# Kernel optimization log

Hardware: AMD Instinct MI355X
Metric: run time of the kernel (lower is better)

Reference implementation:

```python
import jax, jax.numpy as jnp
import numpy as np

WS = 7          # window size
HEADS = 8
SHIFT = WS // 2  # shift=True -> 3
C = 256
KD = C // HEADS  # key_dim = 32
LN_EPS = 1e-3    # keras LayerNormalization default


def setup_inputs() -> dict:
    key = jax.random.key(0)
    ks = jax.random.split(key, 12)
    s = 1.0 / np.sqrt(C)
    x = jax.random.normal(ks[0], (16, 112, 112, C), dtype=jnp.float32)
    wq = jax.random.normal(ks[1], (C, HEADS, KD), dtype=jnp.float32) * s
    bq = jnp.zeros((HEADS, KD), dtype=jnp.float32)
    wk = jax.random.normal(ks[2], (C, HEADS, KD), dtype=jnp.float32) * s
    bk = jnp.zeros((HEADS, KD), dtype=jnp.float32)
    wv = jax.random.normal(ks[3], (C, HEADS, KD), dtype=jnp.float32) * s
    bv = jnp.zeros((HEADS, KD), dtype=jnp.float32)
    wo = jax.random.normal(ks[4], (HEADS, KD, C), dtype=jnp.float32) * s
    bo = jnp.zeros((C,), dtype=jnp.float32)
    gamma = jnp.ones((C,), dtype=jnp.float32)
    beta = jnp.zeros((C,), dtype=jnp.float32)
    return {"x": x, "wq": wq, "bq": bq, "wk": wk, "bk": bk,
            "wv": wv, "bv": bv, "wo": wo, "bo": bo,
            "gamma": gamma, "beta": beta}


def _swin_window_attn(x, wq, bq, wk, bk, wv, bv, wo, bo, gamma, beta):
    b, h, w, c = x.shape
    pad_h = (WS - h % WS) % WS
    pad_w = (WS - w % WS) % WS
    if pad_h or pad_w:
        x = jnp.pad(x, ((0, 0), (0, pad_h), (0, pad_w), (0, 0)))
    hp, wp = h + pad_h, w + pad_w
    if SHIFT > 0:
        x = jnp.roll(x, shift=(-SHIFT, -SHIFT), axis=(1, 2))
    nh, nw = hp // WS, wp // WS
    # window partition: (b, nh, WS, nw, WS, c) -> (b*nh*nw, WS*WS, c)
    win = x.reshape(b, nh, WS, nw, WS, c).transpose(0, 1, 3, 2, 4, 5)
    win = win.reshape(b * nh * nw, WS * WS, c)
    # multi-head attention (keras MHA: query scaled by 1/sqrt(key_dim))
    q = jnp.einsum("nsc,chd->nshd", win, wq) + bq
    k = jnp.einsum("nsc,chd->nshd", win, wk) + bk
    v = jnp.einsum("nsc,chd->nshd", win, wv) + bv
    scores = jnp.einsum("nqhd,nkhd->nhqk", q, k) / jnp.sqrt(jnp.float32(KD)).astype(q.dtype)
    probs = jax.nn.softmax(scores, axis=-1)
    ctx = jnp.einsum("nhqk,nkhd->nqhd", probs, v)
    attn = jnp.einsum("nqhd,hdc->nqc", ctx, wo) + bo
    # residual + LayerNorm
    y = attn + win
    mu = jnp.mean(y, axis=-1, keepdims=True)
    var = jnp.mean(jnp.square(y - mu), axis=-1, keepdims=True)
    y = (y - mu) * jax.lax.rsqrt(var + LN_EPS) * gamma + beta
    # window reverse
    out = y.reshape(b, nh, nw, WS, WS, c).transpose(0, 1, 3, 2, 4, 5)
    out = out.reshape(b, hp, wp, c)
    if SHIFT > 0:
        out = jnp.roll(out, shift=(SHIFT, SHIFT), axis=(1, 2))
    if pad_h or pad_w:
        out = out[:, :h, :w, :]
    return out


def reference(x, wq, bq, wk, bk, wv, bv, wo, bo, gamma, beta):
    return _swin_window_attn(x, wq, bq, wk, bk, wv, bv, wo, bo, gamma, beta)
```

## Files before the change

kernel.cpp:

```cpp
#include <hip/hip_runtime.h>
#include <hip/hip_bf16.h>

typedef __attribute__((ext_vector_type(8))) short short8;
typedef __attribute__((ext_vector_type(4))) short short4v;
typedef __attribute__((ext_vector_type(4))) float float4v;
typedef __attribute__((ext_vector_type(2))) unsigned int uint2v;

#define LDS_BYTES 138272
#define XBF_OFF   0
#define VT_OFF    33792
#define Q_OFF     70656
#define K_OFF     104448
#define CTX_OFF   70656
#define Y_OFF     104448
#define FLAG_OFF  138240

__device__ __forceinline__ unsigned short f2bf_rn(float f) {
    union { __hip_bfloat16 b; unsigned short u; } v;
    v.b = __float2bfloat16(f);
    return v.u;
}
__device__ __forceinline__ unsigned int pk2bf(float a, float b) {
    union { __hip_bfloat162 h; unsigned int u; } v;
    v.h = __float22bfloat162_rn(make_float2(a, b));
    return v.u;
}
__device__ __forceinline__ float bf2f(unsigned short h) {
    union { unsigned int u; float f; } v; v.u = ((unsigned int)h) << 16;
    return v.f;
}
union U8 { unsigned int u[4]; short8 s; };

__global__ void prep_weights(const float* __restrict__ wq, const float* __restrict__ wk,
                             const float* __restrict__ wv, const float* __restrict__ wo,
                             unsigned short* __restrict__ wfrag) {
    int tid = blockIdx.x * 256 + threadIdx.x;
    if (tid >= 4 * 65536) return;
    int m = tid >> 16;
    int e = tid & 65535;
    int j = e & 7;
    int lane = (e >> 3) & 63;
    int nt2 = (e >> 9) & 15;
    int ks = e >> 13;
    int c = ks * 32 + (lane >> 4) * 8 + j;
    int o = nt2 * 16 + (lane & 15);
    const float* W = (m == 0) ? wq : (m == 1) ? wk : (m == 2) ? wv : wo;
    wfrag[tid] = f2bf_rn(W[c * 256 + o]);
}

__global__ __launch_bounds__(1024, 4) void swin_fused(
    const float* __restrict__ x,
    const unsigned short* __restrict__ wfrag,
    const float* __restrict__ bq, const float* __restrict__ bk,
    const float* __restrict__ bv, const float* __restrict__ bo,
    const float* __restrict__ gamma, const float* __restrict__ beta,
    float* __restrict__ out)
{
    extern __shared__ char smem[];
    const int tid = threadIdx.x;
    const int w    = tid >> 6;
    const int h    = w & 7;
    const int half = w >> 3;
    const int l   = tid & 63;
    const int l15 = l & 15;
    const int l4  = l >> 4;
    const int nt2 = 2 * h + half;

    const int blk = blockIdx.x;
    const int bb  = blk >> 8;
    const int wh  = (blk >> 4) & 15;
    const int ww  = blk & 15;

    const unsigned short* wqf = wfrag;
    const unsigned short* wkf = wfrag + 65536;
    const unsigned short* wvf = wfrag + 2 * 65536;
    const int woff0 = (nt2 * 64 + l) * 8;
    short8 bq0 = *(const short8*)(wqf + woff0);
    short8 bk0 = *(const short8*)(wkf + woff0);
    short8 bv0 = *(const short8*)(wvf + woff0);

    unsigned short* Xbf = (unsigned short*)(smem + XBF_OFF);

    if (tid < 8) ((int*)(smem + FLAG_OFF))[tid] = 0;
    for (int idx = tid; idx < 64 * 64; idx += 1024) {
        const int tok = idx >> 6;
        const int c4  = idx & 63;
        float4v f = (float4v){0.f, 0.f, 0.f, 0.f};
        if (tok < 49) {
            const int i = tok / 7;
            const int j = tok - 7 * i;
            int gr = wh * 7 + i + 3; if (gr >= 112) gr -= 112;
            int gc = ww * 7 + j + 3; if (gc >= 112) gc -= 112;
            f = *(const float4v*)(x + (((size_t)bb * 112 + gr) * 112 + gc) * 256 + c4 * 4);
        }
        uint2v u;
        u.x = pk2bf(f.x, f.y);
        u.y = pk2bf(f.z, f.w);
        *(uint2v*)(Xbf + tok * 264 + c4 * 4) = u;
    }
    __syncthreads();

    unsigned short* Qs = (unsigned short*)(smem + Q_OFF);
    unsigned short* Ks = (unsigned short*)(smem + K_OFF);
    unsigned short* Vt = (unsigned short*)(smem + VT_OFF);

    {
        float4v accQ[4], accK[4], accV[4];
#pragma unroll
        for (int mt = 0; mt < 4; ++mt) {
            accQ[mt] = (float4v){0.f, 0.f, 0.f, 0.f};
            accK[mt] = (float4v){0.f, 0.f, 0.f, 0.f};
            accV[mt] = (float4v){0.f, 0.f, 0.f, 0.f};
        }
#pragma unroll
        for (int ks = 0; ks < 8; ++ks) {
            const int woff = ((ks * 16 + nt2) * 64 + l) * 8;
            short8 bq_ = (ks == 0) ? bq0 : *(const short8*)(wqf + woff);
            short8 bk_ = (ks == 0) ? bk0 : *(const short8*)(wkf + woff);
            short8 bv_ = (ks == 0) ? bv0 : *(const short8*)(wvf + woff);
            short8 afr[4];
#pragma unroll
            for (int mt = 0; mt < 4; ++mt)
                afr[mt] = *(const short8*)(Xbf + (mt * 16 + l15) * 264 + ks * 32 + l4 * 8);
            __builtin_amdgcn_s_setprio(1);
#pragma unroll
            for (int mt = 0; mt < 4; ++mt)
                accQ[mt] = __builtin_amdgcn_mfma_f32_16x16x32_bf16(bq_, afr[mt], accQ[mt], 0, 0, 0);
#pragma unroll
            for (int mt = 0; mt < 4; ++mt)
                accK[mt] = __builtin_amdgcn_mfma_f32_16x16x32_bf16(bk_, afr[mt], accK[mt], 0, 0, 0);
#pragma unroll
            for (int mt = 0; mt < 4; ++mt)
                accV[mt] = __builtin_amdgcn_mfma_f32_16x16x32_bf16(afr[mt], bv_, accV[mt], 0, 0, 0);
            __builtin_amdgcn_s_setprio(0);
        }
        const int o0 = nt2 * 16 + 4 * l4;
        const float4v bq4 = *(const float4v*)(bq + o0);
        const float4v bk4 = *(const float4v*)(bk + o0);
#pragma unroll
        for (int mt = 0; mt < 4; ++mt) {
            const int tok = mt * 16 + l15;
            uint2v uq;
            uq.x = pk2bf(accQ[mt][0] + bq4.x, accQ[mt][1] + bq4.y);
            uq.y = pk2bf(accQ[mt][2] + bq4.z, accQ[mt][3] + bq4.w);
            *(uint2v*)(Qs + tok * 264 + o0) = uq;
            uint2v uk;
            uk.x = pk2bf(accK[mt][0] + bk4.x, accK[mt][1] + bk4.y);
            uk.y = pk2bf(accK[mt][2] + bk4.z, accK[mt][3] + bk4.w);
            *(uint2v*)(Ks + tok * 264 + o0) = uk;
        }
        const int o = nt2 * 16 + l15;
        const float biasv = bv[o];
        const int d = half * 16 + l15;
#pragma unroll
        for (int mt = 0; mt < 4; ++mt) {
            uint2v u;
            u.x = pk2bf(accV[mt][0] + biasv, accV[mt][1] + biasv);
            u.y = pk2bf(accV[mt][2] + biasv, accV[mt][3] + biasv);
            *(uint2v*)(Vt + h * 2304 + d * 72 + 32 * (mt >> 1) + 8 * l4 + 4 * (mt & 1)) = u;
        }
    }

    asm volatile("" ::: "memory");
    __threadfence_block();
    if (l == 0) atomicAdd((int*)(smem + FLAG_OFF) + h, 1);
    {
        volatile int* pf = (int*)(smem + FLAG_OFF) + h;
        while (*pf < 2) __builtin_amdgcn_s_sleep(2);
    }
    asm volatile("" ::: "memory");

    const unsigned short* womat = wfrag + 3 * 65536;
    short8 wpre[8];
#pragma unroll
    for (int ks = 0; ks < 8; ++ks)
        wpre[ks] = *(const short8*)(womat + ((ks * 16 + nt2) * 64 + l) * 8);

    float4v sa[4][2];
#pragma unroll
    for (int mt = 0; mt < 4; ++mt)
#pragma unroll
        for (int nt = 0; nt < 2; ++nt)
            sa[mt][nt] = (float4v){0.f, 0.f, 0.f, 0.f};
    {
        short8 kfr[4], qfr[2];
#pragma unroll
        for (int mt = 0; mt < 4; ++mt)
            kfr[mt] = *(const short8*)(Ks + (mt * 16 + l15) * 264 + 32 * h + l4 * 8);
#pragma unroll
        for (int nt = 0; nt < 2; ++nt)
            qfr[nt] = *(const short8*)(Qs + (32 * half + nt * 16 + l15) * 264 + 32 * h + l4 * 8);
        __builtin_amdgcn_s_setprio(1);
#pragma unroll
        for (int mt = 0; mt < 4; ++mt)
#pragma unroll
            for (int nt = 0; nt < 2; ++nt)
                sa[mt][nt] = __builtin_amdgcn_mfma_f32_16x16x32_bf16(kfr[mt], qfr[nt], sa[mt][nt], 0, 0, 0);
        __builtin_amdgcn_s_setprio(0);
    }

    short8 pa[2][2];
    const float SCALE = 0.17677669529663687f;
#pragma unroll
    for (int nt = 0; nt < 2; ++nt) {
        float p[4][4];
        float sum = 0.f;
#pragma unroll
        for (int mt = 0; mt < 4; ++mt)
#pragma unroll
            for (int r = 0; r < 4; ++r) {
                const bool valid = (mt < 3) || ((l4 == 0) && (r == 0));
                const float sv = valid ? sa[mt][nt][r] * SCALE : -1e30f;
                p[mt][r] = __expf(sv);
                sum += p[mt][r];
            }
        sum += __shfl_xor(sum, 16, 64);
        sum += __shfl_xor(sum, 32, 64);
        const float inv = 1.f / sum;
        U8 t0, t1;
        t0.u[0] = pk2bf(p[0][0] * inv, p[0][1] * inv);
        t0.u[1] = pk2bf(p[0][2] * inv, p[0][3] * inv);
        t0.u[2] = pk2bf(p[1][0] * inv, p[1][1] * inv);
        t0.u[3] = pk2bf(p[1][2] * inv, p[1][3] * inv);
        t1.u[0] = pk2bf(p[2][0] * inv, p[2][1] * inv);
        t1.u[1] = pk2bf(p[2][2] * inv, p[2][3] * inv);
        t1.u[2] = pk2bf(p[3][0] * inv, p[3][1] * inv);
        t1.u[3] = pk2bf(p[3][2] * inv, p[3][3] * inv);
        pa[nt][0] = t0.s;
        pa[nt][1] = t1.s;
    }

    float4v cb[2][2];
#pragma unroll
    for (int mtl = 0; mtl < 2; ++mtl)
#pragma unroll
        for (int nt = 0; nt < 2; ++nt)
            cb[mtl][nt] = (float4v){0.f, 0.f, 0.f, 0.f};
#pragma unroll
    for (int ks = 0; ks < 2; ++ks) {
#pragma unroll
        for (int ntv = 0; ntv < 2; ++ntv) {
            short8 vfr = *(const short8*)(Vt + h * 2304 + (ntv * 16 + l15) * 72 + ks * 32 + l4 * 8);
            __builtin_amdgcn_s_setprio(1);
#pragma unroll
            for (int mtl = 0; mtl < 2; ++mtl)
                cb[mtl][ntv] = __builtin_amdgcn_mfma_f32_16x16x32_bf16(vfr, pa[mtl][ks], cb[mtl][ntv], 0, 0, 0);
            __builtin_amdgcn_s_setprio(0);
        }
    }

    unsigned short* Ctx = (unsigned short*)(smem + CTX_OFF);
#pragma unroll
    for (int mtl = 0; mtl < 2; ++mtl) {
        const int tok = 32 * half + mtl * 16 + l15;
#pragma unroll
        for (int ntv = 0; ntv < 2; ++ntv) {
            const int c0 = 32 * h + ntv * 16 + 4 * l4;
            uint2v u;
            u.x = pk2bf(cb[mtl][ntv][0], cb[mtl][ntv][1]);
            u.y = pk2bf(cb[mtl][ntv][2], cb[mtl][ntv][3]);
            *(uint2v*)(Ctx + tok * 264 + c0) = u;
        }
    }
    __syncthreads();

    float4v oa[4];
#pragma unroll
    for (int mt = 0; mt < 4; ++mt) oa[mt] = (float4v){0.f, 0.f, 0.f, 0.f};
#pragma unroll
    for (int ks = 0; ks < 8; ++ks) {
        short8 afr[4];
#pragma unroll
        for (int mt = 0; mt < 4; ++mt)
            afr[mt] = *(const short8*)(Ctx + (mt * 16 + l15) * 264 + ks * 32 + l4 * 8);
        __builtin_amdgcn_s_setprio(1);
#pragma unroll
        for (int mt = 0; mt < 4; ++mt)
            oa[mt] = __builtin_amdgcn_mfma_f32_16x16x32_bf16(wpre[ks], afr[mt], oa[mt], 0, 0, 0);
        __builtin_amdgcn_s_setprio(0);
    }
    unsigned short* Y = (unsigned short*)(smem + Y_OFF);
    {
        const int c0 = nt2 * 16 + 4 * l4;
        const float4v bo4 = *(const float4v*)(bo + c0);
#pragma unroll
        for (int mt = 0; mt < 4; ++mt) {
            const int tok = mt * 16 + l15;
            uint2v u;
            u.x = pk2bf(oa[mt][0] + bo4.x, oa[mt][1] + bo4.y);
            u.y = pk2bf(oa[mt][2] + bo4.z, oa[mt][3] + bo4.w);
            *(uint2v*)(Y + tok * 264 + c0) = u;
        }
    }

    const int lg  = l & 31;
    const int cg0 = lg * 8;
    const float4v g4a  = *(const float4v*)(gamma + cg0);
    const float4v g4b  = *(const float4v*)(gamma + cg0 + 4);
    const float4v be4a = *(const float4v*)(beta  + cg0);
    const float4v be4b = *(const float4v*)(beta  + cg0 + 4);
    __syncthreads();

#pragma unroll
    for (int t = 0; t < 2; ++t) {
        const int tok = 2 * w + (l >> 5) + t * 32;
        if (tok < 49) {
            short8 yr = *(const short8*)(Y + tok * 264 + cg0);
            short8 xr = *(const short8*)(Xbf + tok * 264 + cg0);
            float f[8];
            float sum = 0.f, sq = 0.f;
#pragma unroll
            for (int e = 0; e < 8; ++e) {
                f[e] = bf2f((unsigned short)yr[e]) + bf2f((unsigned short)xr[e]);
                sum += f[e];
                sq  += f[e] * f[e];
            }
#pragma unroll
            for (int msk = 1; msk < 32; msk <<= 1) {
                sum += __shfl_xor(sum, msk, 64);
                sq  += __shfl_xor(sq,  msk, 64);
            }
            const float mu   = sum * (1.f / 256.f);
            const float var  = sq * (1.f / 256.f) - mu * mu;
            const float rstd = rsqrtf(var + 1e-3f);
            const int i = tok / 7;
            const int j = tok - 7 * i;
            int gr = wh * 7 + i + 3; if (gr >= 112) gr -= 112;
            int gc = ww * 7 + j + 3; if (gc >= 112) gc -= 112;
            float* op = out + (((size_t)bb * 112 + gr) * 112 + gc) * 256 + cg0;
            float4v o4a, o4b;
            o4a.x = (f[0] - mu) * rstd * g4a.x + be4a.x;
            o4a.y = (f[1] - mu) * rstd * g4a.y + be4a.y;
            o4a.z = (f[2] - mu) * rstd * g4a.z + be4a.z;
            o4a.w = (f[3] - mu) * rstd * g4a.w + be4a.w;
            o4b.x = (f[4] - mu) * rstd * g4b.x + be4b.x;
            o4b.y = (f[5] - mu) * rstd * g4b.y + be4b.y;
            o4b.z = (f[6] - mu) * rstd * g4b.z + be4b.z;
            o4b.w = (f[7] - mu) * rstd * g4b.w + be4b.w;
            *(float4v*)(op)     = o4a;
            *(float4v*)(op + 4) = o4b;
        }
    }
}

extern "C" void kernel_launch(void* const* d_in, const int* in_sizes, int n_in,
                              void* d_out, int out_size, void* d_ws, size_t ws_size,
                              hipStream_t stream) {
    const float* x     = (const float*)d_in[0];
    const float* wq    = (const float*)d_in[1];
    const float* bq    = (const float*)d_in[2];
    const float* wk    = (const float*)d_in[3];
    const float* bk    = (const float*)d_in[4];
    const float* wv    = (const float*)d_in[5];
    const float* bv    = (const float*)d_in[6];
    const float* wo    = (const float*)d_in[7];
    const float* bo    = (const float*)d_in[8];
    const float* gamma = (const float*)d_in[9];
    const float* beta  = (const float*)d_in[10];
    float* out = (float*)d_out;
    unsigned short* wfrag = (unsigned short*)d_ws;

    prep_weights<<<1024, 256, 0, stream>>>(wq, wk, wv, wo, wfrag);

    hipFuncSetAttribute((const void*)swin_fused,
                        hipFuncAttributeMaxDynamicSharedMemorySize, LDS_BYTES);
    swin_fused<<<4096, 1024, LDS_BYTES, stream>>>(x, wfrag, bq, bk, bv, bo, gamma, beta, out);
}
```

Before: 255.1 us.

## Make blocks persistent over a window row and prefetch next window's input

Each block now loops over the 16 windows of one window-row instead of handling a single window, launching 256 blocks instead of 4096. The next window's input tile is loaded into registers during the current window's output projection and LayerNorm, hiding global load latency. This trades extra per-iteration barriers and serialization within a block for fewer launches and overlapped memory traffic.

```diff
diff --git a/kernel.cpp b/kernel.cpp
--- a/kernel.cpp
+++ b/kernel.cpp
@@ -14,6 +14,7 @@
 #define CTX_OFF   70656
 #define Y_OFF     104448
 #define FLAG_OFF  138240
+#define NW 16
 
 __device__ __forceinline__ unsigned short f2bf_rn(float f) {
     union { __hip_bfloat16 b; unsigned short u; } v;
@@ -67,231 +68,21 @@
     const int nt2 = 2 * h + half;
 
     const int blk = blockIdx.x;
-    const int bb  = blk >> 8;
-    const int wh  = (blk >> 4) & 15;
-    const int ww  = blk & 15;
+    const int bb  = blk >> 4;
+    const int wh  = blk & 15;
 
     const unsigned short* wqf = wfrag;
     const unsigned short* wkf = wfrag + 65536;
     const unsigned short* wvf = wfrag + 2 * 65536;
+    const unsigned short* womat = wfrag + 3 * 65536;
     const int woff0 = (nt2 * 64 + l) * 8;
-    short8 bq0 = *(const short8*)(wqf + woff0);
-    short8 bk0 = *(const short8*)(wkf + woff0);
-    short8 bv0 = *(const short8*)(wvf + woff0);
 
     unsigned short* Xbf = (unsigned short*)(smem + XBF_OFF);
-
-    if (tid < 8) ((int*)(smem + FLAG_OFF))[tid] = 0;
-    for (int idx = tid; idx < 64 * 64; idx += 1024) {
-        const int tok = idx >> 6;
-        const int c4  = idx & 63;
-        float4v f = (float4v){0.f, 0.f, 0.f, 0.f};
-        if (tok < 49) {
-            const int i = tok / 7;
-            const int j = tok - 7 * i;
-            int gr = wh * 7 + i + 3; if (gr >= 112) gr -= 112;
-            int gc = ww * 7 + j + 3; if (gc >= 112) gc -= 112;
-            f = *(const float4v*)(x + (((size_t)bb * 112 + gr) * 112 + gc) * 256 + c4 * 4);
-        }
-        uint2v u;
-        u.x = pk2bf(f.x, f.y);
-        u.y = pk2bf(f.z, f.w);
-        *(uint2v*)(Xbf + tok * 264 + c4 * 4) = u;
-    }
-    __syncthreads();
-
-    unsigned short* Qs = (unsigned short*)(smem + Q_OFF);
-    unsigned short* Ks = (unsigned short*)(smem + K_OFF);
-    unsigned short* Vt = (unsigned short*)(smem + VT_OFF);
-
-    {
-        float4v accQ[4], accK[4], accV[4];
-#pragma unroll
-        for (int mt = 0; mt < 4; ++mt) {
-            accQ[mt] = (float4v){0.f, 0.f, 0.f, 0.f};
-            accK[mt] = (float4v){0.f, 0.f, 0.f, 0.f};
-            accV[mt] = (float4v){0.f, 0.f, 0.f, 0.f};
-        }
-#pragma unroll
-        for (int ks = 0; ks < 8; ++ks) {
-            const int woff = ((ks * 16 + nt2) * 64 + l) * 8;
-            short8 bq_ = (ks == 0) ? bq0 : *(const short8*)(wqf + woff);
-            short8 bk_ = (ks == 0) ? bk0 : *(const short8*)(wkf + woff);
-            short8 bv_ = (ks == 0) ? bv0 : *(const short8*)(wvf + woff);
-            short8 afr[4];
-#pragma unroll
-            for (int mt = 0; mt < 4; ++mt)
-                afr[mt] = *(const short8*)(Xbf + (mt * 16 + l15) * 264 + ks * 32 + l4 * 8);
-            __builtin_amdgcn_s_setprio(1);
-#pragma unroll
-            for (int mt = 0; mt < 4; ++mt)
-                accQ[mt] = __builtin_amdgcn_mfma_f32_16x16x32_bf16(bq_, afr[mt], accQ[mt], 0, 0, 0);
-#pragma unroll
-            for (int mt = 0; mt < 4; ++mt)
-                accK[mt] = __builtin_amdgcn_mfma_f32_16x16x32_bf16(bk_, afr[mt], accK[mt], 0, 0, 0);
-#pragma unroll
-            for (int mt = 0; mt < 4; ++mt)
-                accV[mt] = __builtin_amdgcn_mfma_f32_16x16x32_bf16(afr[mt], bv_, accV[mt], 0, 0, 0);
-            __builtin_amdgcn_s_setprio(0);
-        }
-        const int o0 = nt2 * 16 + 4 * l4;
-        const float4v bq4 = *(const float4v*)(bq + o0);
-        const float4v bk4 = *(const float4v*)(bk + o0);
-#pragma unroll
-        for (int mt = 0; mt < 4; ++mt) {
-            const int tok = mt * 16 + l15;
-            uint2v uq;
-            uq.x = pk2bf(accQ[mt][0] + bq4.x, accQ[mt][1] + bq4.y);
-            uq.y = pk2bf(accQ[mt][2] + bq4.z, accQ[mt][3] + bq4.w);
-            *(uint2v*)(Qs + tok * 264 + o0) = uq;
-            uint2v uk;
-            uk.x = pk2bf(accK[mt][0] + bk4.x, accK[mt][1] + bk4.y);
-            uk.y = pk2bf(accK[mt][2] + bk4.z, accK[mt][3] + bk4.w);
-            *(uint2v*)(Ks + tok * 264 + o0) = uk;
-        }
-        const int o = nt2 * 16 + l15;
-        const float biasv = bv[o];
-        const int d = half * 16 + l15;
-#pragma unroll
-        for (int mt = 0; mt < 4; ++mt) {
-            uint2v u;
-            u.x = pk2bf(accV[mt][0] + biasv, accV[mt][1] + biasv);
-            u.y = pk2bf(accV[mt][2] + biasv, accV[mt][3] + biasv);
-            *(uint2v*)(Vt + h * 2304 + d * 72 + 32 * (mt >> 1) + 8 * l4 + 4 * (mt & 1)) = u;
-        }
-    }
-
-    asm volatile("" ::: "memory");
-    __threadfence_block();
-    if (l == 0) atomicAdd((int*)(smem + FLAG_OFF) + h, 1);
-    {
-        volatile int* pf = (int*)(smem + FLAG_OFF) + h;
-        while (*pf < 2) __builtin_amdgcn_s_sleep(2);
-    }
-    asm volatile("" ::: "memory");
-
-    const unsigned short* womat = wfrag + 3 * 65536;
-    short8 wpre[8];
-#pragma unroll
-    for (int ks = 0; ks < 8; ++ks)
-        wpre[ks] = *(const short8*)(womat + ((ks * 16 + nt2) * 64 + l) * 8);
-
-    float4v sa[4][2];
-#pragma unroll
-    for (int mt = 0; mt < 4; ++mt)
-#pragma unroll
-        for (int nt = 0; nt < 2; ++nt)
-            sa[mt][nt] = (float4v){0.f, 0.f, 0.f, 0.f};
-    {
-        short8 kfr[4], qfr[2];
-#pragma unroll
-        for (int mt = 0; mt < 4; ++mt)
-            kfr[mt] = *(const short8*)(Ks + (mt * 16 + l15) * 264 + 32 * h + l4 * 8);
-#pragma unroll
-        for (int nt = 0; nt < 2; ++nt)
-            qfr[nt] = *(const short8*)(Qs + (32 * half + nt * 16 + l15) * 264 + 32 * h + l4 * 8);
-        __builtin_amdgcn_s_setprio(1);
-#pragma unroll
-        for (int mt = 0; mt < 4; ++mt)
-#pragma unroll
-            for (int nt = 0; nt < 2; ++nt)
-                sa[mt][nt] = __builtin_amdgcn_mfma_f32_16x16x32_bf16(kfr[mt], qfr[nt], sa[mt][nt], 0, 0, 0);
-        __builtin_amdgcn_s_setprio(0);
-    }
-
-    short8 pa[2][2];
-    const float SCALE = 0.17677669529663687f;
-#pragma unroll
-    for (int nt = 0; nt < 2; ++nt) {
-        float p[4][4];
-        float sum = 0.f;
-#pragma unroll
-        for (int mt = 0; mt < 4; ++mt)
-#pragma unroll
-            for (int r = 0; r < 4; ++r) {
-                const bool valid = (mt < 3) || ((l4 == 0) && (r == 0));
-                const float sv = valid ? sa[mt][nt][r] * SCALE : -1e30f;
-                p[mt][r] = __expf(sv);
-                sum += p[mt][r];
-            }
-        sum += __shfl_xor(sum, 16, 64);
-        sum += __shfl_xor(sum, 32, 64);
-        const float inv = 1.f / sum;
-        U8 t0, t1;
-        t0.u[0] = pk2bf(p[0][0] * inv, p[0][1] * inv);
-        t0.u[1] = pk2bf(p[0][2] * inv, p[0][3] * inv);
-        t0.u[2] = pk2bf(p[1][0] * inv, p[1][1] * inv);
-        t0.u[3] = pk2bf(p[1][2] * inv, p[1][3] * inv);
-        t1.u[0] = pk2bf(p[2][0] * inv, p[2][1] * inv);
-        t1.u[1] = pk2bf(p[2][2] * inv, p[2][3] * inv);
-        t1.u[2] = pk2bf(p[3][0] * inv, p[3][1] * inv);
-        t1.u[3] = pk2bf(p[3][2] * inv, p[3][3] * inv);
-        pa[nt][0] = t0.s;
-        pa[nt][1] = t1.s;
-    }
-
-    float4v cb[2][2];
-#pragma unroll
-    for (int mtl = 0; mtl < 2; ++mtl)
-#pragma unroll
-        for (int nt = 0; nt < 2; ++nt)
-            cb[mtl][nt] = (float4v){0.f, 0.f, 0.f, 0.f};
-#pragma unroll
-    for (int ks = 0; ks < 2; ++ks) {
-#pragma unroll
-        for (int ntv = 0; ntv < 2; ++ntv) {
-            short8 vfr = *(const short8*)(Vt + h * 2304 + (ntv * 16 + l15) * 72 + ks * 32 + l4 * 8);
-            __builtin_amdgcn_s_setprio(1);
-#pragma unroll
-            for (int mtl = 0; mtl < 2; ++mtl)
-                cb[mtl][ntv] = __builtin_amdgcn_mfma_f32_16x16x32_bf16(vfr, pa[mtl][ks], cb[mtl][ntv], 0, 0, 0);
-            __builtin_amdgcn_s_setprio(0);
-        }
-    }
-
+    unsigned short* Qs  = (unsigned short*)(smem + Q_OFF);
+    unsigned short* Ks  = (unsigned short*)(smem + K_OFF);
+    unsigned short* Vt  = (unsigned short*)(smem + VT_OFF);
     unsigned short* Ctx = (unsigned short*)(smem + CTX_OFF);
-#pragma unroll
-    for (int mtl = 0; mtl < 2; ++mtl) {
-        const int tok = 32 * half + mtl * 16 + l15;
-#pragma unroll
-        for (int ntv = 0; ntv < 2; ++ntv) {
-            const int c0 = 32 * h + ntv * 16 + 4 * l4;
-            uint2v u;
-            u.x = pk2bf(cb[mtl][ntv][0], cb[mtl][ntv][1]);
-            u.y = pk2bf(cb[mtl][ntv][2], cb[mtl][ntv][3]);
-            *(uint2v*)(Ctx + tok * 264 + c0) = u;
-        }
-    }
-    __syncthreads();
-
-    float4v oa[4];
-#pragma unroll
-    for (int mt = 0; mt < 4; ++mt) oa[mt] = (float4v){0.f, 0.f, 0.f, 0.f};
-#pragma unroll
-    for (int ks = 0; ks < 8; ++ks) {
-        short8 afr[4];
-#pragma unroll
-        for (int mt = 0; mt < 4; ++mt)
-            afr[mt] = *(const short8*)(Ctx + (mt * 16 + l15) * 264 + ks * 32 + l4 * 8);
-        __builtin_amdgcn_s_setprio(1);
-#pragma unroll
-        for (int mt = 0; mt < 4; ++mt)
-            oa[mt] = __builtin_amdgcn_mfma_f32_16x16x32_bf16(wpre[ks], afr[mt], oa[mt], 0, 0, 0);
-        __builtin_amdgcn_s_setprio(0);
-    }
-    unsigned short* Y = (unsigned short*)(smem + Y_OFF);
-    {
-        const int c0 = nt2 * 16 + 4 * l4;
-        const float4v bo4 = *(const float4v*)(bo + c0);
-#pragma unroll
-        for (int mt = 0; mt < 4; ++mt) {
-            const int tok = mt * 16 + l15;
-            uint2v u;
-            u.x = pk2bf(oa[mt][0] + bo4.x, oa[mt][1] + bo4.y);
-            u.y = pk2bf(oa[mt][2] + bo4.z, oa[mt][3] + bo4.w);
-            *(uint2v*)(Y + tok * 264 + c0) = u;
-        }
-    }
+    unsigned short* Y   = (unsigned short*)(smem + Y_OFF);
 
     const int lg  = l & 31;
     const int cg0 = lg * 8;
@@ -299,47 +90,282 @@
     const float4v g4b  = *(const float4v*)(gamma + cg0 + 4);
     const float4v be4a = *(const float4v*)(beta  + cg0);
     const float4v be4b = *(const float4v*)(beta  + cg0 + 4);
-    __syncthreads();
-
-#pragma unroll
-    for (int t = 0; t < 2; ++t) {
-        const int tok = 2 * w + (l >> 5) + t * 32;
+    const int oc0 = nt2 * 16 + 4 * l4;
+    const float4v bq4 = *(const float4v*)(bq + oc0);
+    const float4v bk4 = *(const float4v*)(bk + oc0);
+    const float4v bo4 = *(const float4v*)(bo + oc0);
+    const float biasv = bv[nt2 * 16 + l15];
+
+    if (tid < 8) ((int*)(smem + FLAG_OFF))[tid] = 0;
+
+    const int gr_i = (w < 8) ? -1 : 0;
+    float4v xreg[4];
+#pragma unroll
+    for (int k = 0; k < 4; ++k) {
+        const int tok = w + 16 * k;
+        xreg[k] = (float4v){0.f, 0.f, 0.f, 0.f};
         if (tok < 49) {
-            short8 yr = *(const short8*)(Y + tok * 264 + cg0);
-            short8 xr = *(const short8*)(Xbf + tok * 264 + cg0);
-            float f[8];
-            float sum = 0.f, sq = 0.f;
-#pragma unroll
-            for (int e = 0; e < 8; ++e) {
-                f[e] = bf2f((unsigned short)yr[e]) + bf2f((unsigned short)xr[e]);
-                sum += f[e];
-                sq  += f[e] * f[e];
-            }
-#pragma unroll
-            for (int msk = 1; msk < 32; msk <<= 1) {
-                sum += __shfl_xor(sum, msk, 64);
-                sq  += __shfl_xor(sq,  msk, 64);
-            }
-            const float mu   = sum * (1.f / 256.f);
-            const float var  = sq * (1.f / 256.f) - mu * mu;
-            const float rstd = rsqrtf(var + 1e-3f);
             const int i = tok / 7;
             const int j = tok - 7 * i;
             int gr = wh * 7 + i + 3; if (gr >= 112) gr -= 112;
-            int gc = ww * 7 + j + 3; if (gc >= 112) gc -= 112;
-            float* op = out + (((size_t)bb * 112 + gr) * 112 + gc) * 256 + cg0;
-            float4v o4a, o4b;
-            o4a.x = (f[0] - mu) * rstd * g4a.x + be4a.x;
-            o4a.y = (f[1] - mu) * rstd * g4a.y + be4a.y;
-            o4a.z = (f[2] - mu) * rstd * g4a.z + be4a.z;
-            o4a.w = (f[3] - mu) * rstd * g4a.w + be4a.w;
-            o4b.x = (f[4] - mu) * rstd * g4b.x + be4b.x;
-            o4b.y = (f[5] - mu) * rstd * g4b.y + be4b.y;
-            o4b.z = (f[6] - mu) * rstd * g4b.z + be4b.z;
-            o4b.w = (f[7] - mu) * rstd * g4b.w + be4b.w;
-            *(float4v*)(op)     = o4a;
-            *(float4v*)(op + 4) = o4b;
-        }
+            int gc = 0 * 7 + j + 3;
+            xreg[k] = *(const float4v*)(x + (((size_t)bb * 112 + gr) * 112 + gc) * 256 + l * 4);
+        }
+    }
+
+    for (int it = 0; it < NW; ++it) {
+        const int ww = it;
+
+#pragma unroll
+        for (int k = 0; k < 4; ++k) {
+            const int tok = w + 16 * k;
+            uint2v u;
+            u.x = pk2bf(xreg[k].x, xreg[k].y);
+            u.y = pk2bf(xreg[k].z, xreg[k].w);
+            *(uint2v*)(Xbf + tok * 264 + l * 4) = u;
+        }
+        short8 bq0 = *(const short8*)(wqf + woff0);
+        short8 bk0 = *(const short8*)(wkf + woff0);
+        short8 bv0 = *(const short8*)(wvf + woff0);
+        __syncthreads();
+
+        {
+            float4v accQ[4], accK[4], accV[4];
+#pragma unroll
+            for (int mt = 0; mt < 4; ++mt) {
+                accQ[mt] = (float4v){0.f, 0.f, 0.f, 0.f};
+                accK[mt] = (float4v){0.f, 0.f, 0.f, 0.f};
+                accV[mt] = (float4v){0.f, 0.f, 0.f, 0.f};
+            }
+#pragma unroll
+            for (int ks = 0; ks < 8; ++ks) {
+                const int woff = ((ks * 16 + nt2) * 64 + l) * 8;
+                short8 bq_ = (ks == 0) ? bq0 : *(const short8*)(wqf + woff);
+                short8 bk_ = (ks == 0) ? bk0 : *(const short8*)(wkf + woff);
+                short8 bv_ = (ks == 0) ? bv0 : *(const short8*)(wvf + woff);
+                short8 afr[4];
+#pragma unroll
+                for (int mt = 0; mt < 4; ++mt)
+                    afr[mt] = *(const short8*)(Xbf + (mt * 16 + l15) * 264 + ks * 32 + l4 * 8);
+                __builtin_amdgcn_s_setprio(1);
+#pragma unroll
+                for (int mt = 0; mt < 4; ++mt)
+                    accQ[mt] = __builtin_amdgcn_mfma_f32_16x16x32_bf16(bq_, afr[mt], accQ[mt], 0, 0, 0);
+#pragma unroll
+                for (int mt = 0; mt < 4; ++mt)
+                    accK[mt] = __builtin_amdgcn_mfma_f32_16x16x32_bf16(bk_, afr[mt], accK[mt], 0, 0, 0);
+#pragma unroll
+                for (int mt = 0; mt < 4; ++mt)
+                    accV[mt] = __builtin_amdgcn_mfma_f32_16x16x32_bf16(afr[mt], bv_, accV[mt], 0, 0, 0);
+                __builtin_amdgcn_s_setprio(0);
+            }
+#pragma unroll
+            for (int mt = 0; mt < 4; ++mt) {
+                const int tok = mt * 16 + l15;
+                uint2v uq;
+                uq.x = pk2bf(accQ[mt][0] + bq4.x, accQ[mt][1] + bq4.y);
+                uq.y = pk2bf(accQ[mt][2] + bq4.z, accQ[mt][3] + bq4.w);
+                *(uint2v*)(Qs + tok * 264 + oc0) = uq;
+                uint2v uk;
+                uk.x = pk2bf(accK[mt][0] + bk4.x, accK[mt][1] + bk4.y);
+                uk.y = pk2bf(accK[mt][2] + bk4.z, accK[mt][3] + bk4.w);
+                *(uint2v*)(Ks + tok * 264 + oc0) = uk;
+            }
+            const int d = half * 16 + l15;
+#pragma unroll
+            for (int mt = 0; mt < 4; ++mt) {
+                uint2v u;
+                u.x = pk2bf(accV[mt][0] + biasv, accV[mt][1] + biasv);
+                u.y = pk2bf(accV[mt][2] + biasv, accV[mt][3] + biasv);
+                *(uint2v*)(Vt + h * 2304 + d * 72 + 32 * (mt >> 1) + 8 * l4 + 4 * (mt & 1)) = u;
+            }
+        }
+
+        asm volatile("" ::: "memory");
+        __threadfence_block();
+        if (l == 0) atomicAdd((int*)(smem + FLAG_OFF) + h, 1);
+        {
+            volatile int* pf = (int*)(smem + FLAG_OFF) + h;
+            const int tgt = 2 * (it + 1);
+            while (*pf < tgt) __builtin_amdgcn_s_sleep(2);
+        }
+        asm volatile("" ::: "memory");
+
+        short8 wpre[8];
+#pragma unroll
+        for (int ks = 0; ks < 8; ++ks)
+            wpre[ks] = *(const short8*)(womat + ((ks * 16 + nt2) * 64 + l) * 8);
+
+        float4v sa[4][2];
+#pragma unroll
+        for (int mt = 0; mt < 4; ++mt)
+#pragma unroll
+            for (int nt = 0; nt < 2; ++nt)
+                sa[mt][nt] = (float4v){0.f, 0.f, 0.f, 0.f};
+        {
+            short8 kfr[4], qfr[2];
+#pragma unroll
+            for (int mt = 0; mt < 4; ++mt)
+                kfr[mt] = *(const short8*)(Ks + (mt * 16 + l15) * 264 + 32 * h + l4 * 8);
+#pragma unroll
+            for (int nt = 0; nt < 2; ++nt)
+                qfr[nt] = *(const short8*)(Qs + (32 * half + nt * 16 + l15) * 264 + 32 * h + l4 * 8);
+            __builtin_amdgcn_s_setprio(1);
+#pragma unroll
+            for (int mt = 0; mt < 4; ++mt)
+#pragma unroll
+                for (int nt = 0; nt < 2; ++nt)
+                    sa[mt][nt] = __builtin_amdgcn_mfma_f32_16x16x32_bf16(kfr[mt], qfr[nt], sa[mt][nt], 0, 0, 0);
+            __builtin_amdgcn_s_setprio(0);
+        }
+
+        short8 pa[2][2];
+        const float SCALE = 0.17677669529663687f;
+#pragma unroll
+        for (int nt = 0; nt < 2; ++nt) {
+            float p[4][4];
+            float sum = 0.f;
+#pragma unroll
+            for (int mt = 0; mt < 4; ++mt)
+#pragma unroll
+                for (int r = 0; r < 4; ++r) {
+                    const bool valid = (mt < 3) || ((l4 == 0) && (r == 0));
+                    const float sv = valid ? sa[mt][nt][r] * SCALE : -1e30f;
+                    p[mt][r] = __expf(sv);
+                    sum += p[mt][r];
+                }
+            sum += __shfl_xor(sum, 16, 64);
+            sum += __shfl_xor(sum, 32, 64);
+            const float inv = 1.f / sum;
+            U8 t0, t1;
+            t0.u[0] = pk2bf(p[0][0] * inv, p[0][1] * inv);
+            t0.u[1] = pk2bf(p[0][2] * inv, p[0][3] * inv);
+            t0.u[2] = pk2bf(p[1][0] * inv, p[1][1] * inv);
+            t0.u[3] = pk2bf(p[1][2] * inv, p[1][3] * inv);
+            t1.u[0] = pk2bf(p[2][0] * inv, p[2][1] * inv);
+            t1.u[1] = pk2bf(p[2][2] * inv, p[2][3] * inv);
+            t1.u[2] = pk2bf(p[3][0] * inv, p[3][1] * inv);
+            t1.u[3] = pk2bf(p[3][2] * inv, p[3][3] * inv);
+            pa[nt][0] = t0.s;
+            pa[nt][1] = t1.s;
+        }
+
+        float4v cb[2][2];
+#pragma unroll
+        for (int mtl = 0; mtl < 2; ++mtl)
+#pragma unroll
+            for (int nt = 0; nt < 2; ++nt)
+                cb[mtl][nt] = (float4v){0.f, 0.f, 0.f, 0.f};
+#pragma unroll
+        for (int ks = 0; ks < 2; ++ks) {
+#pragma unroll
+            for (int ntv = 0; ntv < 2; ++ntv) {
+                short8 vfr = *(const short8*)(Vt + h * 2304 + (ntv * 16 + l15) * 72 + ks * 32 + l4 * 8);
+                __builtin_amdgcn_s_setprio(1);
+#pragma unroll
+                for (int mtl = 0; mtl < 2; ++mtl)
+                    cb[mtl][ntv] = __builtin_amdgcn_mfma_f32_16x16x32_bf16(vfr, pa[mtl][ks], cb[mtl][ntv], 0, 0, 0);
+                __builtin_amdgcn_s_setprio(0);
+            }
+        }
+
+#pragma unroll
+        for (int mtl = 0; mtl < 2; ++mtl) {
+            const int tok = 32 * half + mtl * 16 + l15;
+#pragma unroll
+            for (int ntv = 0; ntv < 2; ++ntv) {
+                const int c0 = 32 * h + ntv * 16 + 4 * l4;
+                uint2v u;
+                u.x = pk2bf(cb[mtl][ntv][0], cb[mtl][ntv][1]);
+                u.y = pk2bf(cb[mtl][ntv][2], cb[mtl][ntv][3]);
+                *(uint2v*)(Ctx + tok * 264 + c0) = u;
+            }
+        }
+        __syncthreads();
+
+        float4v oa[4];
+#pragma unroll
+        for (int mt = 0; mt < 4; ++mt) oa[mt] = (float4v){0.f, 0.f, 0.f, 0.f};
+#pragma unroll
+        for (int ks = 0; ks < 8; ++ks) {
+            short8 afr[4];
+#pragma unroll
+            for (int mt = 0; mt < 4; ++mt)
+                afr[mt] = *(const short8*)(Ctx + (mt * 16 + l15) * 264 + ks * 32 + l4 * 8);
+            __builtin_amdgcn_s_setprio(1);
+#pragma unroll
+            for (int mt = 0; mt < 4; ++mt)
+                oa[mt] = __builtin_amdgcn_mfma_f32_16x16x32_bf16(wpre[ks], afr[mt], oa[mt], 0, 0, 0);
+            __builtin_amdgcn_s_setprio(0);
+        }
+        {
+#pragma unroll
+            for (int mt = 0; mt < 4; ++mt) {
+                const int tok = mt * 16 + l15;
+                uint2v u;
+                u.x = pk2bf(oa[mt][0] + bo4.x, oa[mt][1] + bo4.y);
+                u.y = pk2bf(oa[mt][2] + bo4.z, oa[mt][3] + bo4.w);
+                *(uint2v*)(Y + tok * 264 + oc0) = u;
+            }
+        }
+
+        if (it + 1 < NW) {
+#pragma unroll
+            for (int k = 0; k < 4; ++k) {
+                const int tok = w + 16 * k;
+                xreg[k] = (float4v){0.f, 0.f, 0.f, 0.f};
+                if (tok < 49) {
+                    const int i = tok / 7;
+                    const int j = tok - 7 * i;
+                    int gr = wh * 7 + i + 3; if (gr >= 112) gr -= 112;
+                    int gc = (it + 1) * 7 + j + 3; if (gc >= 112) gc -= 112;
+                    xreg[k] = *(const float4v*)(x + (((size_t)bb * 112 + gr) * 112 + gc) * 256 + l * 4);
+                }
+            }
+        }
+        __syncthreads();
+
+#pragma unroll
+        for (int t = 0; t < 2; ++t) {
+            const int tok = 2 * w + (l >> 5) + t * 32;
+            if (tok < 49) {
+                short8 yr = *(const short8*)(Y + tok * 264 + cg0);
+                short8 xr = *(const short8*)(Xbf + tok * 264 + cg0);
+                float f[8];
+                float sum = 0.f, sq = 0.f;
+#pragma unroll
+                for (int e = 0; e < 8; ++e) {
+                    f[e] = bf2f((unsigned short)yr[e]) + bf2f((unsigned short)xr[e]);
+                    sum += f[e];
+                    sq  += f[e] * f[e];
+                }
+#pragma unroll
+                for (int msk = 1; msk < 32; msk <<= 1) {
+                    sum += __shfl_xor(sum, msk, 64);
+                    sq  += __shfl_xor(sq,  msk, 64);
+                }
+                const float mu   = sum * (1.f / 256.f);
+                const float var  = sq * (1.f / 256.f) - mu * mu;
+                const float rstd = rsqrtf(var + 1e-3f);
+                const int i = tok / 7;
+                const int j = tok - 7 * i;
+                int gr = wh * 7 + i + 3; if (gr >= 112) gr -= 112;
+                int gc = ww * 7 + j + 3; if (gc >= 112) gc -= 112;
+                float* op = out + (((size_t)bb * 112 + gr) * 112 + gc) * 256 + cg0;
+                float4v o4a, o4b;
+                o4a.x = (f[0] - mu) * rstd * g4a.x + be4a.x;
+                o4a.y = (f[1] - mu) * rstd * g4a.y + be4a.y;
+                o4a.z = (f[2] - mu) * rstd * g4a.z + be4a.z;
+                o4a.w = (f[3] - mu) * rstd * g4a.w + be4a.w;
+                o4b.x = (f[4] - mu) * rstd * g4b.x + be4b.x;
+                o4b.y = (f[5] - mu) * rstd * g4b.y + be4b.y;
+                o4b.z = (f[6] - mu) * rstd * g4b.z + be4b.z;
+                o4b.w = (f[7] - mu) * rstd * g4b.w + be4b.w;
+                *(float4v*)(op)     = o4a;
+                *(float4v*)(op + 4) = o4b;
+            }
+        }
+        __syncthreads();
     }
 }
 
@@ -364,5 +390,5 @@
 
     hipFuncSetAttribute((const void*)swin_fused,
                         hipFuncAttributeMaxDynamicSharedMemorySize, LDS_BYTES);
-    swin_fused<<<4096, 1024, LDS_BYTES, stream>>>(x, wfrag, bq, bk, bv, bo, gamma, beta, out);
-}
+    swin_fused<<<256, 1024, LDS_BYTES, stream>>>(x, wfrag, bq, bk, bv, bo, gamma, beta, out);
+}
```

After: 603.6 us. 137% more time.
